# Kernel optimization log

Measured on AMD Instinct MI355X. Metric: run time of the kernel, lower is better.

## Reference

```python
import math
import jax, jax.numpy as jnp
import numpy as np

L, B, D = 2048, 8, 1024
Z, H, N = 128, 2048, 16


def setup_inputs() -> dict:
    key = jax.random.key(0)
    ks = jax.random.split(key, 16)
    s = 0.02
    inp = {
        "x": jax.random.normal(ks[0], (L, B, D), jnp.float32),
        "ln_w": jnp.ones((D,), jnp.float32),
        "ln_b": jnp.zeros((D,), jnp.float32),
        "v_w": jax.random.normal(ks[1], (H, D), jnp.float32) * s,
        "v_b": jnp.zeros((H,), jnp.float32),
        "mx_w": jax.random.normal(ks[2], (Z + H + 2 * D, D), jnp.float32) * s,
        "mx_b": jnp.zeros((Z + H + 2 * D,), jnp.float32),
        "h_w": jax.random.normal(ks[3], (D, H), jnp.float32) * s,
        "h_b": jnp.zeros((D,), jnp.float32),
        "qk_gamma": jnp.ones((2, Z), jnp.float32) + jax.random.normal(ks[4], (2, Z), jnp.float32) * s,
        "qk_beta": jax.random.normal(ks[5], (2, Z), jnp.float32) * s,
        "ema_delta": jax.random.normal(ks[6], (D, N, 1), jnp.float32),
        "ema_alpha": jax.random.normal(ks[7], (D, N, 1), jnp.float32),
        "ema_beta": jax.random.normal(ks[8], (D, N, 1), jnp.float32) * s,
        "ema_gamma": jax.random.normal(ks[9], (D, N), jnp.float32) * s,
        "ema_omega": jax.random.normal(ks[10], (D,), jnp.float32) * s,
        "rb_alpha": jax.random.normal(ks[11], (1, Z), jnp.float32) * s,
        "rb_beta": jax.random.normal(ks[12], (1, Z), jnp.float32) * s,
    }
    return inp


def _rotary_bias(rb_alpha, rb_beta, seq_len, z):
    # RotaryRelativePositionalBias.forward(seq_len) -> (L, L)
    half = z // 2
    freqs = jnp.exp(jnp.arange(half, dtype=jnp.float32) * (-math.log(10000.0) / half))
    pos = jnp.arange(seq_len, dtype=jnp.float32)[:, None] * freqs[None, :]  # (L, half)
    sin, cos = jnp.sin(pos), jnp.cos(pos)

    def rot(w):  # (1, Z) -> (L, Z)
        we = jnp.broadcast_to(w, (seq_len, z))
        w1, w2 = we[:, :half], we[:, half:]
        return jnp.concatenate([w1 * cos - w2 * sin, w2 * cos + w1 * sin], axis=1)

    return rot(rb_alpha) @ rot(rb_beta).T  # (L, L)


def _ema(xn, ema_delta, ema_alpha, ema_beta, ema_gamma, ema_omega):
    # xn: (L, B, D) -> damped multi-head EMA via FFT causal conv (MEGA MultiHeadEMA)
    seq_len = xn.shape[0]
    p = jax.nn.sigmoid(ema_delta)           # (D, N, 1)
    a = jax.nn.sigmoid(ema_alpha)           # (D, N, 1)
    q = 1.0 - p * a                         # (D, N, 1)
    t = jnp.arange(seq_len, dtype=jnp.float32)[None, None, :]
    kern = (p * ema_beta) * jnp.exp(t * jnp.log(q))          # (D, N, L)
    scale = math.sqrt(1.0 / kern.shape[1])
    k_dl = jnp.einsum("dnl,dn->dl", kern, ema_gamma * scale)  # (D, L)
    xt = jnp.transpose(xn, (1, 2, 0))        # (B, D, L)
    nfft = 2 * seq_len
    kf = jnp.fft.rfft(k_dl, n=nfft)          # (D, F)
    xf = jnp.fft.rfft(xt, n=nfft)            # (B, D, F)
    conv = jnp.fft.irfft(xf * kf, n=nfft)[..., :seq_len]      # (B, D, L)
    return jax.nn.silu(jnp.transpose(conv, (2, 0, 1)) + xn * ema_omega)  # (L, B, D)


def reference(x, ln_w, ln_b, v_w, v_b, mx_w, mx_b, h_w, h_b, qk_gamma, qk_beta,
              ema_delta, ema_alpha, ema_beta, ema_gamma, ema_omega, rb_alpha, rb_beta):
    seq_len, bsz, d = x.shape
    residual = x
    # prenorm LayerNorm
    mu = jnp.mean(x, axis=-1, keepdims=True)
    var = jnp.mean(jnp.square(x - mu), axis=-1, keepdims=True)
    xn = (x - mu) * jax.lax.rsqrt(var + 1e-5) * ln_w + ln_b

    v = jax.nn.silu(xn @ v_w.T + v_b)                          # (L, B, H)
    mx = _ema(xn, ema_delta, ema_alpha, ema_beta, ema_gamma, ema_omega)
    base = mx @ mx_w.T + mx_b                                  # (L, B, Z+H+2D)
    u = jax.nn.sigmoid(base[..., :d])                          # update gate
    zr = jax.nn.silu(base[..., d:d + Z + H])
    hx = base[..., d + Z + H:]
    z, r = zr[..., :Z], zr[..., Z:]                            # (L,B,Z), (L,B,H)
    z2 = z[:, :, None, :] * qk_gamma + qk_beta                 # (L, B, 2, Z)
    q = jnp.transpose(z2[:, :, 0], (1, 0, 2)) * (Z ** -0.5)    # (B, L, Z)
    k = jnp.transpose(z2[:, :, 1], (1, 0, 2))                  # (B, L, Z)
    vb = jnp.transpose(v, (1, 0, 2))                           # (B, L, H)

    bias = _rotary_bias(rb_alpha, rb_beta, seq_len, Z)         # (L, L)
    attn = jax.nn.softmax(jnp.einsum("blz,bmz->blm", q, k) + bias, axis=-1)
    h = jnp.transpose(jnp.einsum("blm,bmh->blh", attn, vb), (1, 0, 2))  # (L, B, H)
    h = jax.nn.silu(hx + (h * r) @ h_w.T + h_b)                # (L, B, D)
    return residual + u * (h - residual)
```

## Files before the change

kernel.cpp:

```cpp
#include <hip/hip_runtime.h>
#include <cstdint>
#include <cstddef>

typedef __bf16 bf16;
typedef __bf16 bf16x8 __attribute__((ext_vector_type(8)));
typedef float  f32x4  __attribute__((ext_vector_type(4)));

#define DEVI static __device__ __forceinline__

DEVI float fsigmoid(float x) { return 1.0f / (1.0f + __expf(-x)); }
DEVI float fsilu(float x)    { return x / (1.0f + __expf(-x)); }

DEVI unsigned short b16bits(float v) { bf16 h = (bf16)v; return __builtin_bit_cast(unsigned short, h); }
DEVI float lo16f(unsigned int w) { return __builtin_bit_cast(float, w << 16); }
DEVI float hi16f(unsigned int w) { return __builtin_bit_cast(float, w & 0xffff0000u); }

DEVI float waveRedSum(float v) {
#pragma unroll
  for (int o = 32; o > 0; o >>= 1) v += __shfl_xor(v, o, 64);
  return v;
}
DEVI float waveRedMax(float v) {
#pragma unroll
  for (int o = 32; o > 0; o >>= 1) v = fmaxf(v, __shfl_xor(v, o, 64));
  return v;
}

DEVI void xcd_swizzle(int& bx, int& by) {
  const int gx = gridDim.x, gy = gridDim.y;
  const int nwg = gx * gy;
  const int flat = blockIdx.y * gx + blockIdx.x;
  const int xcd = flat & 7;
  const int rem = nwg & 7;
  const int q = nwg >> 3;
  const int base = (xcd < rem) ? xcd * (q + 1) : rem * (q + 1) + (xcd - rem) * q;
  const int swz = base + (flat >> 3);
  bx = swz % gx;
  by = swz / gx;
}

struct alignas(8) B4 { bf16 x, y, z, w; };

__global__ __launch_bounds__(256) void k_copyout(const float* __restrict__ x, float* __restrict__ o)
{
  const long i = (long)blockIdx.x * 256 + threadIdx.x;
  ((float4*)o)[i] = ((const float4*)x)[i];
}

__global__ __launch_bounds__(256) void k_lnstats(const float* __restrict__ x, float* __restrict__ stats)
{
  const long t = blockIdx.x;
  const int tid = threadIdx.x;
  const float4 v = ((const float4*)(x + t * 1024))[tid];
  float s  = v.x + v.y + v.z + v.w;
  float s2 = v.x * v.x + v.y * v.y + v.z * v.z + v.w * v.w;
  __shared__ float red[2][4];
  s = waveRedSum(s);
  s2 = waveRedSum(s2);
  const int wv = tid >> 6, ln = tid & 63;
  if (ln == 0) { red[0][wv] = s; red[1][wv] = s2; }
  __syncthreads();
  if (tid == 0) {
    s  = red[0][0] + red[0][1] + red[0][2] + red[0][3];
    s2 = red[1][0] + red[1][1] + red[1][2] + red[1][3];
    const float mu  = s * (1.0f / 1024.0f);
    const float var = s2 * (1.0f / 1024.0f) - mu * mu;
    stats[2 * t]     = mu;
    stats[2 * t + 1] = rsqrtf(var + 1e-5f);
  }
}

__global__ __launch_bounds__(256) void k_cvt(const float* __restrict__ in, bf16* __restrict__ out, int n4)
{
  const int i = blockIdx.x * 256 + threadIdx.x;
  if (i >= n4) return;
  const float4 v = ((const float4*)in)[i];
  B4 h; h.x = (bf16)v.x; h.y = (bf16)v.y; h.z = (bf16)v.z; h.w = (bf16)v.w;
  ((B4*)out)[i] = h;
}

__global__ __launch_bounds__(256) void k_ema_coeff(
    const float* __restrict__ de, const float* __restrict__ al,
    const float* __restrict__ be, const float* __restrict__ ga,
    float* __restrict__ qv, float* __restrict__ cv)
{
  const int i = blockIdx.x * 256 + threadIdx.x;
  const int d = i >> 4, n = i & 15;
  const float p = 1.0f / (1.0f + expf(-de[i]));
  const float a = 1.0f / (1.0f + expf(-al[i]));
  qv[n * 1024 + d] = 1.0f - p * a;
  cv[n * 1024 + d] = p * be[i] * ga[i] * 0.25f;
}

__global__ __launch_bounds__(256) void k_ema_scan1(
    const float* __restrict__ x, const float* __restrict__ stats,
    const float* __restrict__ lnw, const float* __restrict__ lnb,
    const float* __restrict__ qv, float* __restrict__ scan)
{
  const int d = blockIdx.x * 256 + threadIdx.x;
  const int b = blockIdx.y, c = blockIdx.z;
  float q[16], s[16];
#pragma unroll
  for (int n = 0; n < 16; ++n) { q[n] = qv[n * 1024 + d]; s[n] = 0.0f; }
  const float wd = lnw[d], bd = lnb[d];
  const float* xp = x + (long)b * 1024 + d;
  const int l0 = c * 128;
  for (int j0 = 0; j0 < 128; j0 += 8) {
    float xr[8]; float2 st[8];
#pragma unroll
    for (int i = 0; i < 8; ++i) {
      const int l = l0 + j0 + i;
      xr[i] = xp[(long)l * 8192];
      st[i] = ((const float2*)stats)[(long)l * 8 + b];
    }
#pragma unroll
    for (int i = 0; i < 8; ++i) {
      const float xv = (xr[i] - st[i].x) * st[i].y * wd + bd;
#pragma unroll
      for (int n = 0; n < 16; ++n) s[n] = fmaf(q[n], s[n], xv);
    }
  }
  float* sp = scan + ((((long)c * 8 + b) * 1024) + d) * 16;
#pragma unroll
  for (int n = 0; n < 16; ++n) sp[n] = s[n];
}

__global__ __launch_bounds__(256) void k_ema_scan2(
    const float* __restrict__ qv, float* __restrict__ scan)
{
  const int i = blockIdx.x * 256 + threadIdx.x;
  const int n = i & 15, d = (i >> 4) & 1023, b = i >> 14;
  const float q = qv[n * 1024 + d];
  const float q2 = q * q, q4 = q2 * q2, q8 = q4 * q4;
  const float q16 = q8 * q8, q32 = q16 * q16, q64 = q32 * q32, q128 = q64 * q64;
  float carry = 0.0f;
#pragma unroll
  for (int c = 0; c < 16; ++c) {
    const long off = ((((long)c * 8 + b) * 1024) + d) * 16 + n;
    const float t = scan[off];
    scan[off] = carry;
    carry = fmaf(q128, carry, t);
  }
}

__global__ __launch_bounds__(256) void k_ema_apply(
    const float* __restrict__ x, const float* __restrict__ stats,
    const float* __restrict__ lnw, const float* __restrict__ lnb,
    const float* __restrict__ qv, const float* __restrict__ cv,
    const float* __restrict__ omega, const float* __restrict__ scan,
    bf16* __restrict__ mx)
{
  const int d = blockIdx.x * 256 + threadIdx.x;
  const int b = blockIdx.y, c = blockIdx.z;
  float q[16], cc[16], s[16];
  const float* sp = scan + ((((long)c * 8 + b) * 1024) + d) * 16;
#pragma unroll
  for (int n = 0; n < 16; ++n) {
    q[n] = qv[n * 1024 + d];
    cc[n] = cv[n * 1024 + d];
    s[n] = sp[n];
  }
  const float om = omega[d], wd = lnw[d], bd = lnb[d];
  const float* xp = x + (long)b * 1024 + d;
  bf16* mp = mx + (long)b * 1024 + d;
  const int l0 = c * 128;
  for (int j0 = 0; j0 < 128; j0 += 8) {
    float xr[8]; float2 st[8];
#pragma unroll
    for (int i = 0; i < 8; ++i) {
      const int l = l0 + j0 + i;
      xr[i] = xp[(long)l * 8192];
      st[i] = ((const float2*)stats)[(long)l * 8 + b];
    }
#pragma unroll
    for (int i = 0; i < 8; ++i) {
      const float xv = (xr[i] - st[i].x) * st[i].y * wd + bd;
      float p0 = 0.f, p1 = 0.f, p2 = 0.f, p3 = 0.f;
#pragma unroll
      for (int n = 0; n < 16; n += 4) {
        s[n]     = fmaf(q[n],     s[n],     xv);
        s[n + 1] = fmaf(q[n + 1], s[n + 1], xv);
        s[n + 2] = fmaf(q[n + 2], s[n + 2], xv);
        s[n + 3] = fmaf(q[n + 3], s[n + 3], xv);
        p0 = fmaf(cc[n],     s[n],     p0);
        p1 = fmaf(cc[n + 1], s[n + 1], p1);
        p2 = fmaf(cc[n + 2], s[n + 2], p2);
        p3 = fmaf(cc[n + 3], s[n + 3], p3);
      }
      const float pre = fmaf(xv, om, (p0 + p1) + (p2 + p3));
      mp[(long)(l0 + j0 + i) * 8192] = (bf16)fsilu(pre);
    }
  }
}

__global__ __launch_bounds__(64) void k_rotfill(
    const float* __restrict__ rba, const float* __restrict__ rbb,
    bf16* __restrict__ Qp, bf16* __restrict__ Kp)
{
  const int l = blockIdx.x, zi = threadIdx.x;
  const float fr = __expf(-0.14391156831212787f * (float)zi);
  const float pos = (float)l * fr;
  const float sn = sinf(pos), cs = cosf(pos);
  const float a1 = rba[zi], a2 = rba[64 + zi];
  const float b1 = rbb[zi], b2 = rbb[64 + zi];
  const bf16 qa = (bf16)(a1 * cs - a2 * sn);
  const bf16 qb = (bf16)(a2 * cs + a1 * sn);
  const bf16 ka = (bf16)(b1 * cs - b2 * sn);
  const bf16 kb = (bf16)(b2 * cs + b1 * sn);
#pragma unroll
  for (int b = 0; b < 8; ++b) {
    const long base = ((long)b * 2048 + l) * 256;
    Qp[base + 128 + zi] = qa;
    Qp[base + 192 + zi] = qb;
    Kp[base + 128 + zi] = ka;
    Kp[base + 192 + zi] = kb;
  }
}

__global__ __launch_bounds__(256) void k_softmax(float* __restrict__ S)
{
  const long row = blockIdx.x;
  float* sp = S + row * 2048;
  const int tid = threadIdx.x;
  float vals[8];
  float mx = -1e30f;
#pragma unroll
  for (int i = 0; i < 8; ++i) { vals[i] = sp[i * 256 + tid]; mx = fmaxf(mx, vals[i]); }
  __shared__ float red[4];
  mx = waveRedMax(mx);
  const int wv = tid >> 6, ln = tid & 63;
  if (ln == 0) red[wv] = mx;
  __syncthreads();
  mx = fmaxf(fmaxf(red[0], red[1]), fmaxf(red[2], red[3]));
  float sum = 0.f;
#pragma unroll
  for (int i = 0; i < 8; ++i) { vals[i] = __expf(vals[i] - mx); sum += vals[i]; }
  __syncthreads();
  sum = waveRedSum(sum);
  if (ln == 0) red[wv] = sum;
  __syncthreads();
  sum = red[0] + red[1] + red[2] + red[3];
  const float inv = 1.0f / sum;
  bf16* pp = (bf16*)sp;
#pragma unroll
  for (int i = 0; i < 8; ++i) pp[i * 256 + tid] = (bf16)(vals[i] * inv);
}

__global__ __launch_bounds__(1024) void k_vtrans8(
    const bf16* __restrict__ v, bf16* __restrict__ vt, const int loff)
{
  __shared__ bf16 tile[32][33];
  const int l0 = blockIdx.x * 32, h0 = blockIdx.y * 32, b = blockIdx.z;
  const int tx = threadIdx.x, ty = threadIdx.y;
  tile[ty][tx] = v[((long)(l0 + ty) * 8 + b) * 2048 + h0 + tx];
  __syncthreads();
  vt[((long)b * 2048 + h0 + ty) * 2048 + loff + l0 + tx] = tile[tx][ty];
}

DEVI void gload16(const void* g, void* l) {
  __builtin_amdgcn_global_load_lds(
      (__attribute__((address_space(1))) void*)(void*)g,
      (__attribute__((address_space(3))) void*)l, 16, 0, 0);
}

DEVI void drain_vmem() {
  asm volatile("s_waitcnt vmcnt(0)" ::: "memory");
}

template<int EPI>
__global__ __launch_bounds__(512, 2) void k_gemm256(
    const bf16* __restrict__ A, const bf16* __restrict__ Bm,
    const int K, const int lda, const int ldb, const int ncols,
    const float* __restrict__ bias,
    void* __restrict__ o0, void* __restrict__ o1, void* __restrict__ o2, void* __restrict__ o3,
    const void* __restrict__ e0, const void* __restrict__ e1)
{
  __shared__ alignas(16) bf16 As[2][16384];
  __shared__ alignas(16) bf16 Bs[2][16384];
  const int tid = threadIdx.x;
  const int wid = tid >> 6, lane = tid & 63;
  const int wm = wid >> 2, wn = wid & 3;
  int bx, by;
  xcd_swizzle(bx, by);
  const int tm = by * 256, tn = bx * 256;
  const int fr = lane & 15, kg = lane >> 4;
  const int swR = (fr & 7) << 3;

  f32x4 acc[8][4];
  const f32x4 z4 = {0.0f, 0.0f, 0.0f, 0.0f};
#pragma unroll
  for (int i = 0; i < 8; ++i)
#pragma unroll
    for (int j = 0; j < 4; ++j) acc[i][j] = z4;

  int srow[4], scolv[4];
#pragma unroll
  for (int g = 0; g < 4; ++g) {
    const int cidx = g * 512 + tid;
    srow[g] = cidx >> 3;
    scolv[g] = ((cidx & 7) ^ (srow[g] & 7)) * 8;
  }

  const int nt = K >> 6;
#pragma unroll
  for (int g = 0; g < 4; ++g) {
    gload16(A + (long)(tm + srow[g]) * lda + scolv[g], &As[0][g * 4096 + wid * 512]);
    gload16(Bm + (long)(tn + srow[g]) * ldb + scolv[g], &Bs[0][g * 4096 + wid * 512]);
  }
  drain_vmem();
  __syncthreads();

  for (int t = 0; t < nt; ++t) {
    const int cur = t & 1;
    if (t + 1 < nt) {
      const int k1 = (t + 1) << 6;
#pragma unroll
      for (int g = 0; g < 4; ++g) {
        gload16(A + (long)(tm + srow[g]) * lda + k1 + scolv[g], &As[cur ^ 1][g * 4096 + wid * 512]);
        gload16(Bm + (long)(tn + srow[g]) * ldb + k1 + scolv[g], &Bs[cur ^ 1][g * 4096 + wid * 512]);
      }
    }
    const bf16* Ab = &As[cur][0];
    const bf16* Bb = &Bs[cur][0];
#pragma unroll
    for (int ks = 0; ks < 2; ++ks) {
      bf16x8 af[8], bfv[4];
#pragma unroll
      for (int j = 0; j < 4; ++j)
        bfv[j] = *(const bf16x8*)&Bb[(wn * 64 + j * 16 + fr) * 64 + ((ks * 32 + kg * 8) ^ swR)];
#pragma unroll
      for (int i = 0; i < 8; ++i)
        af[i] = *(const bf16x8*)&Ab[(wm * 128 + i * 16 + fr) * 64 + ((ks * 32 + kg * 8) ^ swR)];
#pragma unroll
      for (int i = 0; i < 8; ++i)
#pragma unroll
        for (int j = 0; j < 4; ++j)
          acc[i][j] = __builtin_amdgcn_mfma_f32_16x16x32_bf16(af[i], bfv[j], acc[i][j], 0, 0, 0);
    }
    drain_vmem();
    __syncthreads();
  }

#pragma unroll
  for (int i = 0; i < 8; ++i) {
#pragma unroll
    for (int j = 0; j < 4; ++j) {
#pragma unroll
      for (int rr = 0; rr < 4; ++rr) {
        const int row = tm + wm * 128 + i * 16 + kg * 4 + rr;
        const int col = tn + wn * 64 + j * 16 + fr;
        const float a = acc[i][j][rr];
        if constexpr (EPI == 1) {
          if (col >= ncols) continue;
          const float tv = a + bias[col];
          if (col < 1024) {
            ((unsigned short*)o0)[((long)row * 1024 + col) * 2] = b16bits(fsigmoid(tv));
          } else if (col < 1152) {
            const int zi = col - 1024;
            const float zval = fsilu(tv);
            const float qq = (zval * ((const float*)e0)[zi] + ((const float*)e1)[zi]) * 0.08838834764831845f;
            const float kk =  zval * ((const float*)e0)[128 + zi] + ((const float*)e1)[128 + zi];
            const long base = ((long)(row & 7) * 2048 + (row >> 3)) * 256 + zi;
            ((bf16*)o2)[base] = (bf16)qq;
            ((bf16*)o3)[base] = (bf16)kk;
          } else if (col < 3200) {
            ((bf16*)o1)[(long)row * 2048 + (col - 1152)] = (bf16)fsilu(tv);
          } else {
            ((unsigned short*)o0)[((long)row * 1024 + (col - 3200)) * 2 + 1] = b16bits(tv);
          }
        } else if constexpr (EPI == 4) {
          const long idx = (long)row * 1024 + col;
          const unsigned int w = ((const unsigned int*)o0)[idx];
          const float uv = lo16f(w), hxv = hi16f(w);
          const float hval = fsilu(hxv + a + bias[col]);
          const float xv = ((const float*)e1)[idx];
          ((float*)o0)[idx] = xv + uv * (hval - xv);
        }
      }
    }
  }
}

template<int EPI>
__global__ __launch_bounds__(256) void k_gemm_bt(
    const bf16* __restrict__ A, const bf16* __restrict__ Bm,
    const int K, const int lda, const int ldb, const int coladd,
    const float* __restrict__ bias,
    void* __restrict__ o0, void* __restrict__ o1, void* __restrict__ o2, void* __restrict__ o3,
    const void* __restrict__ e0, const void* __restrict__ e1, const void* __restrict__ e2)
{
  __shared__ alignas(16) bf16 As[128 * 64];
  __shared__ alignas(16) bf16 Bs[128 * 64];
  const int tid = threadIdx.x;
  const int wave = tid >> 6, lane = tid & 63;
  const int wm = wave >> 1, wn = wave & 1;
  int bx, by;
  xcd_swizzle(bx, by);
  const int tm = by * 128, tn = bx * 128;
  const int fr = lane & 15, kg = lane >> 4;

  f32x4 acc[4][4];
  const f32x4 z4 = {0.0f, 0.0f, 0.0f, 0.0f};
#pragma unroll
  for (int i = 0; i < 4; ++i)
#pragma unroll
    for (int j = 0; j < 4; ++j) acc[i][j] = z4;

  const int srow = wave * 8 + (lane >> 3);
  const int scol = ((lane & 7) ^ (lane >> 3)) * 8;
  const long arow = (long)(tm + srow);
  const long brow = (long)(tn + srow);
  const int swR = (fr & 7) << 3;

  for (int k0 = 0; k0 < K; k0 += 64) {
    __syncthreads();
#pragma unroll
    for (int cc = 0; cc < 4; ++cc) {
      gload16(A + (arow + cc * 32) * lda + k0 + scol, As + cc * 2048 + wave * 512);
      gload16(Bm + (brow + cc * 32) * ldb + k0 + scol, Bs + cc * 2048 + wave * 512);
    }
    __syncthreads();
    bf16x8 af[2][4], bfv[2][4];
#pragma unroll
    for (int ks = 0; ks < 2; ++ks)
#pragma unroll
      for (int i = 0; i < 4; ++i) {
        af[ks][i]  = *(const bf16x8*)&As[(wm * 64 + i * 16 + fr) * 64 + ((ks * 32 + kg * 8) ^ swR)];
        bfv[ks][i] = *(const bf16x8*)&Bs[(wn * 64 + i * 16 + fr) * 64 + ((ks * 32 + kg * 8) ^ swR)];
      }
#pragma unroll
    for (int ks = 0; ks < 2; ++ks)
#pragma unroll
      for (int i = 0; i < 4; ++i)
#pragma unroll
        for (int j = 0; j < 4; ++j)
          acc[i][j] = __builtin_amdgcn_mfma_f32_16x16x32_bf16(af[ks][i], bfv[ks][j], acc[i][j], 0, 0, 0);
  }

#pragma unroll
  for (int i = 0; i < 4; ++i) {
#pragma unroll
    for (int j = 0; j < 4; ++j) {
#pragma unroll
      for (int rr = 0; rr < 4; ++rr) {
        const int row = tm + wm * 64 + i * 16 + kg * 4 + rr;
        const int col = coladd + tn + wn * 64 + j * 16 + fr;
        const float a = acc[i][j][rr];
        if constexpr (EPI == 2) {
          ((float*)o0)[(long)row * 2048 + col] = a;
        } else if constexpr (EPI == 3) {
          const long idx = (long)row * 16384 + col;
          const float rv = (float)((const bf16*)e0)[idx];
          ((bf16*)o0)[idx] = (bf16)(a * rv);
        }
      }
    }
  }
}

__global__ __launch_bounds__(256) void k_gemm_lnA(
    const float* __restrict__ x, const float* __restrict__ stats,
    const float* __restrict__ lnw, const float* __restrict__ lnb,
    const bf16* __restrict__ Bm, const float* __restrict__ bias,
    bf16* __restrict__ out)
{
  __shared__ alignas(16) bf16 As[128 * 64];
  __shared__ alignas(16) bf16 Bs[128 * 64];
  __shared__ float smu[128], srs[128];
  const int tid = threadIdx.x;
  const int wave = tid >> 6, lane = tid & 63;
  const int wm = wave >> 1, wn = wave & 1;
  int bx, by;
  xcd_swizzle(bx, by);
  const int tm = by * 128, tn = bx * 128;
  const int fr = lane & 15, kg = lane >> 4;
  if (tid < 128) {
    smu[tid] = stats[2 * (long)(tm + tid)];
    srs[tid] = stats[2 * (long)(tm + tid) + 1];
  }

  f32x4 acc[4][4];
  const f32x4 z4 = {0.0f, 0.0f, 0.0f, 0.0f};
#pragma unroll
  for (int i = 0; i < 4; ++i)
#pragma unroll
    for (int j = 0; j < 4; ++j) acc[i][j] = z4;

  const int srow = wave * 8 + (lane >> 3);
  const int scol = ((lane & 7) ^ (lane >> 3)) * 8;
  const long brow = (long)(tn + srow);
  const int swR = (fr & 7) << 3;
  const int ar = tid & 127, ah = (tid >> 7) * 32;
  const float* xrow = x + (long)(tm + ar) * 1024 + ah;

  for (int k0 = 0; k0 < 1024; k0 += 64) {
    __syncthreads();
#pragma unroll
    for (int cc = 0; cc < 4; ++cc)
      gload16(Bm + (brow + cc * 32) * 1024 + k0 + scol, Bs + cc * 2048 + wave * 512);
    {
      const float mu = smu[ar], rs = srs[ar];
      bf16 tmp[32];
#pragma unroll
      for (int i = 0; i < 8; ++i) {
        const float4 xv = ((const float4*)(xrow + k0))[i];
        const float4 wv = ((const float4*)(lnw + k0 + ah))[i];
        const float4 bv = ((const float4*)(lnb + k0 + ah))[i];
        tmp[i * 4 + 0] = (bf16)((xv.x - mu) * rs * wv.x + bv.x);
        tmp[i * 4 + 1] = (bf16)((xv.y - mu) * rs * wv.y + bv.y);
        tmp[i * 4 + 2] = (bf16)((xv.z - mu) * rs * wv.z + bv.z);
        tmp[i * 4 + 3] = (bf16)((xv.w - mu) * rs * wv.w + bv.w);
      }
      const int sw = (ar & 7) << 3;
#pragma unroll
      for (int i = 0; i < 4; ++i)
        *(bf16x8*)&As[ar * 64 + ((ah + i * 8) ^ sw)] = *(const bf16x8*)&tmp[i * 8];
    }
    __syncthreads();
    bf16x8 af[2][4], bfv[2][4];
#pragma unroll
    for (int ks = 0; ks < 2; ++ks)
#pragma unroll
      for (int i = 0; i < 4; ++i) {
        const int ar2 = wm * 64 + i * 16 + fr;
        af[ks][i]  = *(const bf16x8*)&As[ar2 * 64 + ((ks * 32 + kg * 8) ^ ((ar2 & 7) << 3))];
        bfv[ks][i] = *(const bf16x8*)&Bs[(wn * 64 + i * 16 + fr) * 64 + ((ks * 32 + kg * 8) ^ swR)];
      }
#pragma unroll
    for (int ks = 0; ks < 2; ++ks)
#pragma unroll
      for (int i = 0; i < 4; ++i)
#pragma unroll
        for (int j = 0; j < 4; ++j)
          acc[i][j] = __builtin_amdgcn_mfma_f32_16x16x32_bf16(af[ks][i], bfv[ks][j], acc[i][j], 0, 0, 0);
  }

#pragma unroll
  for (int i = 0; i < 4; ++i)
#pragma unroll
    for (int j = 0; j < 4; ++j)
#pragma unroll
      for (int rr = 0; rr < 4; ++rr) {
        const int row = tm + wm * 64 + i * 16 + kg * 4 + rr;
        const int col = tn + wn * 64 + j * 16 + fr;
        out[(long)row * 2048 + col] = (bf16)fsilu(acc[i][j][rr] + bias[col]);
      }
}

extern "C" void kernel_launch(void* const* d_in, const int* in_sizes, int n_in,
                              void* d_out, int out_size, void* d_ws, size_t ws_size,
                              hipStream_t stream)
{
  const float* x    = (const float*)d_in[0];
  const float* ln_w = (const float*)d_in[1];
  const float* ln_b = (const float*)d_in[2];
  const float* v_w  = (const float*)d_in[3];
  const float* v_b  = (const float*)d_in[4];
  const float* mx_w = (const float*)d_in[5];
  const float* mx_b = (const float*)d_in[6];
  const float* h_w  = (const float*)d_in[7];
  const float* h_b  = (const float*)d_in[8];
  const float* qk_g = (const float*)d_in[9];
  const float* qk_b = (const float*)d_in[10];
  const float* e_de = (const float*)d_in[11];
  const float* e_al = (const float*)d_in[12];
  const float* e_be = (const float*)d_in[13];
  const float* e_ga = (const float*)d_in[14];
  const float* e_om = (const float*)d_in[15];
  const float* rb_a = (const float*)d_in[16];
  const float* rb_b = (const float*)d_in[17];

  const size_t MiB = 1048576UL;
  if (ws_size < 160 * MiB) {
    k_copyout<<<16384, 256, 0, stream>>>(x, (float*)d_out);
    return;
  }

  char* ws = (char*)d_ws;
  bf16*  rbuf  = (bf16*)(ws + 0 * MiB);
  bf16*  v_t   = (bf16*)(ws + 64 * MiB);
  bf16*  mxw_h = (bf16*)(ws + 64 * MiB);
  bf16*  mxb   = (bf16*)(ws + 73 * MiB);
  float* qv    = (float*)(ws + 105 * MiB);
  float* cv    = (float*)(ws + 105 * MiB + 65536);
  bf16*  Qp    = (bf16*)(ws + 128 * MiB);
  bf16*  hw_h  = (bf16*)(ws + 128 * MiB);
  bf16*  Kp    = (bf16*)(ws + 136 * MiB);
  float* Sbuf  = (float*)(ws + 144 * MiB);
  bf16*  vw_h  = (bf16*)(ws + 144 * MiB);
  float* scanb = (float*)(ws + 148 * MiB);
  bf16*  vbufe = (bf16*)(ws + 148 * MiB);
  float* stats = (float*)(ws + 156 * MiB);

  k_lnstats<<<16384, 256, 0, stream>>>(x, stats);
  k_cvt<<<2048, 256, 0, stream>>>(v_w, vw_h, 524288);
  hipMemsetAsync(mxw_h + 4224L * 1024, 0, 128L * 1024 * 2, stream);
  k_cvt<<<4224, 256, 0, stream>>>(mx_w, mxw_h, 1081344);
  k_ema_coeff<<<64, 256, 0, stream>>>(e_de, e_al, e_be, e_ga, qv, cv);

  k_ema_scan1<<<dim3(4, 8, 16), 256, 0, stream>>>(x, stats, ln_w, ln_b, qv, scanb);
  k_ema_scan2<<<512, 256, 0, stream>>>(qv, scanb);
  k_ema_apply<<<dim3(4, 8, 16), 256, 0, stream>>>(x, stats, ln_w, ln_b, qv, cv, e_om, scanb, mxb);

  k_gemm256<1><<<dim3(17, 64, 1), 512, 0, stream>>>(mxb, mxw_h, 1024, 1024, 1024, 4224,
      mx_b, d_out, (void*)rbuf, (void*)Qp, (void*)Kp, (const void*)qk_g, (const void*)qk_b);
  k_rotfill<<<2048, 64, 0, stream>>>(rb_a, rb_b, Qp, Kp);

  for (int e = 0; e < 8; ++e) {
    k_gemm_lnA<<<dim3(16, 16, 1), 256, 0, stream>>>(x + (long)e * 2048 * 1024, stats + (long)e * 4096,
        ln_w, ln_b, vw_h, v_b, vbufe);
    k_vtrans8<<<dim3(8, 64, 8), dim3(32, 32), 0, stream>>>(vbufe, v_t, e * 256);
  }

  for (int b = 0; b < 8; ++b) {
    const bf16* Ab = Qp + (long)b * 524288;
    const bf16* Bb = Kp + (long)b * 524288;
    k_gemm_bt<2><<<dim3(16, 16, 1), 256, 0, stream>>>(Ab, Bb, 256, 256, 256, 0,
        nullptr, (void*)Sbuf, nullptr, nullptr, nullptr, nullptr, nullptr, nullptr);
    k_softmax<<<2048, 256, 0, stream>>>(Sbuf);
    bf16* hrp = rbuf + (long)b * 2048;
    k_gemm_bt<3><<<dim3(16, 16, 1), 256, 0, stream>>>((const bf16*)Sbuf, v_t + (long)b * 4194304,
        2048, 4096, 2048, 0, nullptr, (void*)hrp, nullptr, nullptr, nullptr, (const void*)hrp, nullptr, nullptr);
  }

  k_cvt<<<2048, 256, 0, stream>>>(h_w, hw_h, 524288);

  k_gemm256<4><<<dim3(4, 64, 1), 512, 0, stream>>>(rbuf, hw_h, 2048, 2048, 2048, 1024,
      h_b, d_out, nullptr, nullptr, nullptr, nullptr, (const void*)x);
}
```

Measured before the change: 1.540 ms.

## Replace 256x256 double-buffered GEMM with 128x128 four-stage pipelined GEMM

Replaces the 512-thread 256x256-tile GEMM with a 256-thread 128x128-tile kernel that keeps four LDS stages and issues loads three K-steps ahead. Partial vmcnt waits replace the full drain, so global loads stay in flight while MFMAs run. The same kernel now also serves the attention-times-V GEMM, where it replaces k_gemm_bt. Smaller tiles give more blocks on the large GEMMs, at the cost of less reuse per block. The mx GEMM grid now exactly covers 4224 columns, so the column guard and the memset of padding rows are removed.

```diff
diff --git a/kernel.cpp b/kernel.cpp
--- a/kernel.cpp
+++ b/kernel.cpp
@@ -263,95 +263,90 @@
       (__attribute__((address_space(3))) void*)l, 16, 0, 0);
 }
 
-DEVI void drain_vmem() {
-  asm volatile("s_waitcnt vmcnt(0)" ::: "memory");
-}
-
 template<int EPI>
-__global__ __launch_bounds__(512, 2) void k_gemm256(
+__global__ __launch_bounds__(256) void k_gemm_p3(
     const bf16* __restrict__ A, const bf16* __restrict__ Bm,
-    const int K, const int lda, const int ldb, const int ncols,
+    const int K, const int lda, const int ldb,
     const float* __restrict__ bias,
     void* __restrict__ o0, void* __restrict__ o1, void* __restrict__ o2, void* __restrict__ o3,
     const void* __restrict__ e0, const void* __restrict__ e1)
 {
-  __shared__ alignas(16) bf16 As[2][16384];
-  __shared__ alignas(16) bf16 Bs[2][16384];
+  __shared__ alignas(16) bf16 As[4][8192];
+  __shared__ alignas(16) bf16 Bs[4][8192];
   const int tid = threadIdx.x;
-  const int wid = tid >> 6, lane = tid & 63;
-  const int wm = wid >> 2, wn = wid & 3;
+  const int wave = tid >> 6, lane = tid & 63;
+  const int wm = wave >> 1, wn = wave & 1;
   int bx, by;
   xcd_swizzle(bx, by);
-  const int tm = by * 256, tn = bx * 256;
+  const int tm = by * 128, tn = bx * 128;
   const int fr = lane & 15, kg = lane >> 4;
   const int swR = (fr & 7) << 3;
 
-  f32x4 acc[8][4];
+  f32x4 acc[4][4];
   const f32x4 z4 = {0.0f, 0.0f, 0.0f, 0.0f};
 #pragma unroll
-  for (int i = 0; i < 8; ++i)
+  for (int i = 0; i < 4; ++i)
 #pragma unroll
     for (int j = 0; j < 4; ++j) acc[i][j] = z4;
 
-  int srow[4], scolv[4];
-#pragma unroll
-  for (int g = 0; g < 4; ++g) {
-    const int cidx = g * 512 + tid;
-    srow[g] = cidx >> 3;
-    scolv[g] = ((cidx & 7) ^ (srow[g] & 7)) * 8;
-  }
+  const int srow = wave * 8 + (lane >> 3);
+  const int scol = ((lane & 7) ^ (lane >> 3)) * 8;
+  const long arow = (long)(tm + srow);
+  const long brow = (long)(tn + srow);
+
+#define STAGE_P3(buf, kt) do { const int k0_ = (kt) << 6;                                   \
+    _Pragma("unroll")                                                                        \
+    for (int cc_ = 0; cc_ < 4; ++cc_) {                                                      \
+      gload16(A  + (arow + cc_ * 32) * lda + k0_ + scol, &As[buf][cc_ * 2048 + wave * 512]); \
+      gload16(Bm + (brow + cc_ * 32) * ldb + k0_ + scol, &Bs[buf][cc_ * 2048 + wave * 512]); \
+    } } while (0)
 
   const int nt = K >> 6;
-#pragma unroll
-  for (int g = 0; g < 4; ++g) {
-    gload16(A + (long)(tm + srow[g]) * lda + scolv[g], &As[0][g * 4096 + wid * 512]);
-    gload16(Bm + (long)(tn + srow[g]) * ldb + scolv[g], &Bs[0][g * 4096 + wid * 512]);
-  }
-  drain_vmem();
+  STAGE_P3(0, 0);
+  STAGE_P3(1, 1);
+  STAGE_P3(2, 2);
+  asm volatile("s_waitcnt vmcnt(16)" ::: "memory");
   __syncthreads();
 
   for (int t = 0; t < nt; ++t) {
-    const int cur = t & 1;
-    if (t + 1 < nt) {
-      const int k1 = (t + 1) << 6;
-#pragma unroll
-      for (int g = 0; g < 4; ++g) {
-        gload16(A + (long)(tm + srow[g]) * lda + k1 + scolv[g], &As[cur ^ 1][g * 4096 + wid * 512]);
-        gload16(Bm + (long)(tn + srow[g]) * ldb + k1 + scolv[g], &Bs[cur ^ 1][g * 4096 + wid * 512]);
-      }
-    }
+    const int cur = t & 3;
+    if (t + 3 < nt) STAGE_P3((t + 3) & 3, t + 3);
     const bf16* Ab = &As[cur][0];
     const bf16* Bb = &Bs[cur][0];
-#pragma unroll
-    for (int ks = 0; ks < 2; ++ks) {
-      bf16x8 af[8], bfv[4];
-#pragma unroll
-      for (int j = 0; j < 4; ++j)
-        bfv[j] = *(const bf16x8*)&Bb[(wn * 64 + j * 16 + fr) * 64 + ((ks * 32 + kg * 8) ^ swR)];
-#pragma unroll
-      for (int i = 0; i < 8; ++i)
-        af[i] = *(const bf16x8*)&Ab[(wm * 128 + i * 16 + fr) * 64 + ((ks * 32 + kg * 8) ^ swR)];
-#pragma unroll
-      for (int i = 0; i < 8; ++i)
+    bf16x8 af[2][4], bfv[2][4];
+#pragma unroll
+    for (int ks = 0; ks < 2; ++ks)
+#pragma unroll
+      for (int i = 0; i < 4; ++i) {
+        af[ks][i]  = *(const bf16x8*)&Ab[(wm * 64 + i * 16 + fr) * 64 + ((ks * 32 + kg * 8) ^ swR)];
+        bfv[ks][i] = *(const bf16x8*)&Bb[(wn * 64 + i * 16 + fr) * 64 + ((ks * 32 + kg * 8) ^ swR)];
+      }
+#pragma unroll
+    for (int ks = 0; ks < 2; ++ks)
+#pragma unroll
+      for (int i = 0; i < 4; ++i)
 #pragma unroll
         for (int j = 0; j < 4; ++j)
-          acc[i][j] = __builtin_amdgcn_mfma_f32_16x16x32_bf16(af[i], bfv[j], acc[i][j], 0, 0, 0);
-    }
-    drain_vmem();
-    __syncthreads();
-  }
-
-#pragma unroll
-  for (int i = 0; i < 8; ++i) {
+          acc[i][j] = __builtin_amdgcn_mfma_f32_16x16x32_bf16(af[ks][i], bfv[ks][j], acc[i][j], 0, 0, 0);
+    if (t + 1 < nt) {
+      if (t + 3 < nt)      asm volatile("s_waitcnt vmcnt(16)" ::: "memory");
+      else if (t + 2 < nt) asm volatile("s_waitcnt vmcnt(8)"  ::: "memory");
+      else                 asm volatile("s_waitcnt vmcnt(0)"  ::: "memory");
+      __syncthreads();
+    }
+  }
+#undef STAGE_P3
+
+#pragma unroll
+  for (int i = 0; i < 4; ++i) {
 #pragma unroll
     for (int j = 0; j < 4; ++j) {
 #pragma unroll
       for (int rr = 0; rr < 4; ++rr) {
-        const int row = tm + wm * 128 + i * 16 + kg * 4 + rr;
+        const int row = tm + wm * 64 + i * 16 + kg * 4 + rr;
         const int col = tn + wn * 64 + j * 16 + fr;
         const float a = acc[i][j][rr];
         if constexpr (EPI == 1) {
-          if (col >= ncols) continue;
           const float tv = a + bias[col];
           if (col < 1024) {
             ((unsigned short*)o0)[((long)row * 1024 + col) * 2] = b16bits(fsigmoid(tv));
@@ -368,6 +363,10 @@
           } else {
             ((unsigned short*)o0)[((long)row * 1024 + (col - 3200)) * 2 + 1] = b16bits(tv);
           }
+        } else if constexpr (EPI == 3) {
+          const long idx = (long)row * 16384 + col;
+          const float rv = (float)((const bf16*)e0)[idx];
+          ((bf16*)o0)[idx] = (bf16)(a * rv);
         } else if constexpr (EPI == 4) {
           const long idx = (long)row * 1024 + col;
           const unsigned int w = ((const unsigned int*)o0)[idx];
@@ -448,10 +447,6 @@
         const float a = acc[i][j][rr];
         if constexpr (EPI == 2) {
           ((float*)o0)[(long)row * 2048 + col] = a;
-        } else if constexpr (EPI == 3) {
-          const long idx = (long)row * 16384 + col;
-          const float rv = (float)((const bf16*)e0)[idx];
-          ((bf16*)o0)[idx] = (bf16)(a * rv);
         }
       }
     }
@@ -594,7 +589,6 @@
 
   k_lnstats<<<16384, 256, 0, stream>>>(x, stats);
   k_cvt<<<2048, 256, 0, stream>>>(v_w, vw_h, 524288);
-  hipMemsetAsync(mxw_h + 4224L * 1024, 0, 128L * 1024 * 2, stream);
   k_cvt<<<4224, 256, 0, stream>>>(mx_w, mxw_h, 1081344);
   k_ema_coeff<<<64, 256, 0, stream>>>(e_de, e_al, e_be, e_ga, qv, cv);
 
@@ -602,7 +596,7 @@
   k_ema_scan2<<<512, 256, 0, stream>>>(qv, scanb);
   k_ema_apply<<<dim3(4, 8, 16), 256, 0, stream>>>(x, stats, ln_w, ln_b, qv, cv, e_om, scanb, mxb);
 
-  k_gemm256<1><<<dim3(17, 64, 1), 512, 0, stream>>>(mxb, mxw_h, 1024, 1024, 1024, 4224,
+  k_gemm_p3<1><<<dim3(33, 128, 1), 256, 0, stream>>>(mxb, mxw_h, 1024, 1024, 1024,
       mx_b, d_out, (void*)rbuf, (void*)Qp, (void*)Kp, (const void*)qk_g, (const void*)qk_b);
   k_rotfill<<<2048, 64, 0, stream>>>(rb_a, rb_b, Qp, Kp);
 
@@ -619,12 +613,12 @@
         nullptr, (void*)Sbuf, nullptr, nullptr, nullptr, nullptr, nullptr, nullptr);
     k_softmax<<<2048, 256, 0, stream>>>(Sbuf);
     bf16* hrp = rbuf + (long)b * 2048;
-    k_gemm_bt<3><<<dim3(16, 16, 1), 256, 0, stream>>>((const bf16*)Sbuf, v_t + (long)b * 4194304,
-        2048, 4096, 2048, 0, nullptr, (void*)hrp, nullptr, nullptr, nullptr, (const void*)hrp, nullptr, nullptr);
+    k_gemm_p3<3><<<dim3(16, 16, 1), 256, 0, stream>>>((const bf16*)Sbuf, v_t + (long)b * 4194304,
+        2048, 4096, 2048, nullptr, (void*)hrp, nullptr, nullptr, nullptr, (const void*)hrp, nullptr);
   }
 
   k_cvt<<<2048, 256, 0, stream>>>(h_w, hw_h, 524288);
 
-  k_gemm256<4><<<dim3(4, 64, 1), 512, 0, stream>>>(rbuf, hw_h, 2048, 2048, 2048, 1024,
+  k_gemm_p3<4><<<dim3(8, 128, 1), 256, 0, stream>>>(rbuf, hw_h, 2048, 2048, 2048,
       h_b, d_out, nullptr, nullptr, nullptr, nullptr, (const void*)x);
 }
```

Result: no change. 1.565 ms (+1.6%).
